# Performance work log

Hardware: AMD Instinct MI355X
Metric: run time of the kernel (lower is better)

The kernel has to match this reference:

```python
import jax, jax.numpy as jnp
import numpy as np


def _mk_mat(rows):
    # rows: list of 3 lists of (B,) arrays, written as matrix rows.
    # torch code stacks rows at dim=2, which transposes: replicate that.
    M = jnp.stack([jnp.stack(r, axis=1) for r in rows], axis=1)  # (B,3,3) written-rows
    return jnp.swapaxes(M, 1, 2)  # matches torch.stack(..., dim=2)


def _compose_mats(affine, scale, translate, shear):
    B = affine.shape[0]
    one = jnp.ones((B,), affine.dtype)
    zero = jnp.zeros((B,), affine.dtype)
    cx, sx = jnp.cos(affine[:, 0]), jnp.sin(affine[:, 0])
    cy, sy = jnp.cos(affine[:, 1]), jnp.sin(affine[:, 1])
    cz, sz = jnp.cos(affine[:, 2]), jnp.sin(affine[:, 2])
    rot_x = _mk_mat([[one, zero, zero], [zero, cx, -sx], [zero, sx, cx]])
    rot_y = _mk_mat([[cy, zero, sy], [zero, one, zero], [-sy, zero, cy]])
    rot_z = _mk_mat([[cz, -sz, zero], [sz, cz, zero], [zero, zero, one]])
    scale_m = _mk_mat([[scale[:, 0], zero, zero], [zero, scale[:, 1], zero], [zero, zero, scale[:, 2]]])
    t = jnp.tan(shear)
    shear_m = _mk_mat([[one, t[:, 0], t[:, 1]], [t[:, 2], one, t[:, 3]], [t[:, 4], t[:, 5], one]])
    trans = translate[:, :, None]  # (B,3,1)
    mat3 = shear_m @ (scale_m @ (rot_z @ (rot_y @ rot_x)))  # (B,3,3)
    inv3 = jnp.linalg.inv(mat3)
    mat = jnp.concatenate([mat3, trans], axis=-1)  # (B,3,4)
    inv_trans = jnp.matmul(-inv3, trans)
    inv_mat = jnp.concatenate([inv3, inv_trans], axis=-1)
    return mat, inv_mat


def _affine_grid(mat, D, H, W):
    # torch affine_grid, align_corners=False: coord_i = (2*i+1)/n - 1
    dt = mat.dtype
    xs = (jnp.arange(W, dtype=dt) + 0.5) * (2.0 / W) - 1.0
    ys = (jnp.arange(H, dtype=dt) + 0.5) * (2.0 / H) - 1.0
    zs = (jnp.arange(D, dtype=dt) + 0.5) * (2.0 / D) - 1.0
    zz, yy, xx = jnp.meshgrid(zs, ys, xs, indexing='ij')
    coords = jnp.stack([xx, yy, zz], axis=-1)  # (D,H,W,3) in (x,y,z) order
    grid = jnp.einsum('bkj,dhwj->bdhwk', mat[:, :, :3], coords) + mat[:, None, None, None, :, 3]
    return grid  # (B,D,H,W,3)


def _grid_sample_trilinear(src, grid):
    # torch grid_sample, mode='bilinear' (trilinear in 3D), padding zeros, align_corners=False
    B, C, D, H, W = src.shape
    ix = (grid[..., 0] + 1.0) * (W * 0.5) - 0.5
    iy = (grid[..., 1] + 1.0) * (H * 0.5) - 0.5
    iz = (grid[..., 2] + 1.0) * (D * 0.5) - 0.5
    fx, fy, fz = jnp.floor(ix), jnp.floor(iy), jnp.floor(iz)
    wx, wy, wz = ix - fx, iy - fy, iz - fz  # fractional weights
    x0, y0, z0 = fx.astype(jnp.int32), fy.astype(jnp.int32), fz.astype(jnp.int32)
    x1, y1, z1 = x0 + 1, y0 + 1, z0 + 1
    N = D * H * W
    src_flat = src.reshape(B, C, N)

    def gather(z, y, x):
        valid = (x >= 0) & (x < W) & (y >= 0) & (y < H) & (z >= 0) & (z < D)
        xi = jnp.clip(x, 0, W - 1)
        yi = jnp.clip(y, 0, H - 1)
        zi = jnp.clip(z, 0, D - 1)
        idx = ((zi * H + yi) * W + xi).reshape(B, 1, N)
        v = jnp.take_along_axis(src_flat, jnp.broadcast_to(idx, (B, C, N)), axis=2)
        return v * valid.reshape(B, 1, N).astype(src.dtype)

    def w(a):
        return a.reshape(B, 1, N)

    out = (gather(z0, y0, x0) * w((1 - wz) * (1 - wy) * (1 - wx))
           + gather(z0, y0, x1) * w((1 - wz) * (1 - wy) * wx)
           + gather(z0, y1, x0) * w((1 - wz) * wy * (1 - wx))
           + gather(z0, y1, x1) * w((1 - wz) * wy * wx)
           + gather(z1, y0, x0) * w(wz * (1 - wy) * (1 - wx))
           + gather(z1, y0, x1) * w(wz * (1 - wy) * wx)
           + gather(z1, y1, x0) * w(wz * wy * (1 - wx))
           + gather(z1, y1, x1) * w(wz * wy * wx))
    return out.reshape(B, C, D, H, W)


def setup_inputs() -> dict:
    key = jax.random.key(0)
    k1, k2, k3, k4, k5 = jax.random.split(key, 5)
    B, C, D, H, W = 2, 1, 192, 192, 192
    src = jax.random.normal(k1, (B, C, D, H, W), dtype=jnp.float32)
    affine = jax.random.uniform(k2, (B, 3), dtype=jnp.float32)
    scale = jax.random.uniform(k3, (B, 3), dtype=jnp.float32)
    translate = jax.random.uniform(k4, (B, 3), dtype=jnp.float32)
    shear = jax.random.uniform(k5, (B, 6), dtype=jnp.float32)
    return {"src": src, "affine": affine, "scale": scale, "translate": translate, "shear": shear}


def reference(src, affine, scale, translate, shear):
    B, C, D, H, W = src.shape
    mat, inv_mat = _compose_mats(affine, scale, translate, shear)
    grid = _affine_grid(mat, D, H, W)
    warped = _grid_sample_trilinear(src, grid)
    return warped, mat, inv_mat
```

## Files before the change

### kernel.cpp

```cpp
#include <hip/hip_runtime.h>
#include <math.h>

#define Bv 2
#define Dv 192
#define Hv 192
#define Wv 192
#define Nv (Dv*Hv*Wv)
#define NOUT (Bv*Nv)

#define TLZ 8
#define SWID 32
#define CAPF 13312

typedef float v2f __attribute__((ext_vector_type(2)));

__device__ __forceinline__ void mm3(const float a[3][3], const float b[3][3], float c[3][3]) {
#pragma unroll
    for (int i = 0; i < 3; ++i)
#pragma unroll
        for (int j = 0; j < 3; ++j)
            c[i][j] = a[i][0]*b[0][j] + a[i][1]*b[1][j] + a[i][2]*b[2][j];
}

__global__ void compose_mats_kernel(const float* __restrict__ affine,
                                    const float* __restrict__ scale,
                                    const float* __restrict__ translate,
                                    const float* __restrict__ shear,
                                    float* __restrict__ mats_out) {
    int b = threadIdx.x;
    if (b >= Bv) return;

    float ax = affine[b*3+0], ay = affine[b*3+1], az = affine[b*3+2];
    float cx = cosf(ax), sx = sinf(ax);
    float cy = cosf(ay), sy = sinf(ay);
    float cz = cosf(az), sz = sinf(az);

    float rx[3][3] = {{1.f,0.f,0.f},{0.f,cx,sx},{0.f,-sx,cx}};
    float ry[3][3] = {{cy,0.f,-sy},{0.f,1.f,0.f},{sy,0.f,cy}};
    float rz[3][3] = {{cz,sz,0.f},{-sz,cz,0.f},{0.f,0.f,1.f}};

    float t0 = tanf(shear[b*6+0]), t1 = tanf(shear[b*6+1]), t2 = tanf(shear[b*6+2]);
    float t3 = tanf(shear[b*6+3]), t4 = tanf(shear[b*6+4]), t5 = tanf(shear[b*6+5]);
    float sh[3][3] = {{1.f,t2,t4},{t0,1.f,t5},{t1,t3,1.f}};

    float s0 = scale[b*3+0], s1 = scale[b*3+1], s2 = scale[b*3+2];

    float m1[3][3], m2[3][3], m3s[3][3], mat3[3][3];
    mm3(ry, rx, m1);
    mm3(rz, m1, m2);
#pragma unroll
    for (int j = 0; j < 3; ++j) { m3s[0][j] = s0*m2[0][j]; m3s[1][j] = s1*m2[1][j]; m3s[2][j] = s2*m2[2][j]; }
    mm3(sh, m3s, mat3);

    float tr0 = translate[b*3+0], tr1 = translate[b*3+1], tr2 = translate[b*3+2];

    float a00 = mat3[0][0], a01 = mat3[0][1], a02 = mat3[0][2];
    float a10 = mat3[1][0], a11 = mat3[1][1], a12 = mat3[1][2];
    float a20 = mat3[2][0], a21 = mat3[2][1], a22 = mat3[2][2];
    float c00 =  (a11*a22 - a12*a21);
    float c01 = -(a10*a22 - a12*a20);
    float c02 =  (a10*a21 - a11*a20);
    float det = a00*c00 + a01*c01 + a02*c02;
    float rdet = 1.0f / det;
    float inv3[3][3];
    inv3[0][0] = c00*rdet;
    inv3[0][1] = (a02*a21 - a01*a22)*rdet;
    inv3[0][2] = (a01*a12 - a02*a11)*rdet;
    inv3[1][0] = c01*rdet;
    inv3[1][1] = (a00*a22 - a02*a20)*rdet;
    inv3[1][2] = (a02*a10 - a00*a12)*rdet;
    inv3[2][0] = c02*rdet;
    inv3[2][1] = (a01*a20 - a00*a21)*rdet;
    inv3[2][2] = (a00*a11 - a01*a10)*rdet;

    float* mo = mats_out + b*12;
#pragma unroll
    for (int i = 0; i < 3; ++i) {
        mo[i*4+0] = mat3[i][0]; mo[i*4+1] = mat3[i][1]; mo[i*4+2] = mat3[i][2];
    }
    mo[0*4+3] = tr0; mo[1*4+3] = tr1; mo[2*4+3] = tr2;

    float* io = mats_out + 24 + b*12;
#pragma unroll
    for (int i = 0; i < 3; ++i) {
        io[i*4+0] = inv3[i][0]; io[i*4+1] = inv3[i][1]; io[i*4+2] = inv3[i][2];
        io[i*4+3] = -(inv3[i][0]*tr0 + inv3[i][1]*tr1 + inv3[i][2]*tr2);
    }
}

__device__ __forceinline__ float2 ld2(const float* p) {
    float2 r;
    __builtin_memcpy(&r, p, 8);
    return r;
}

__device__ __forceinline__ void gld_lds4(const float* g, float* l) {
    __builtin_amdgcn_global_load_lds(
        (const __attribute__((address_space(1))) unsigned int*)g,
        (__attribute__((address_space(3))) unsigned int*)l, 4, 0, 0);
}

__global__ __launch_bounds__(512) void warp_kernel(const float* __restrict__ src,
                                                   const float* __restrict__ mats,
                                                   float* __restrict__ out) {
    __shared__ float stage[CAPF];

    int t   = threadIdx.x;
    int lx  = t & 15;
    int ly  = (t >> 4) & 15;
    int lzt = t >> 8;

    int W0 = blockIdx.x * 16;
    int H0 = blockIdx.y * 16;
    int zt = blockIdx.z;
    int b  = zt / (Dv/TLZ);
    int Z0 = (zt % (Dv/TLZ)) * TLZ;

    const float* M = mats + b*12;
    float m00 = M[0], m01 = M[1],  m02 = M[2],  m03 = M[3];
    float m10 = M[4], m11 = M[5],  m12 = M[6],  m13 = M[7];
    float m20 = M[8], m21 = M[9],  m22 = M[10], m23 = M[11];

    float Cx = 96.0f*(m03 - m00 - m01 - m02) + 95.5f;
    float Cy = 96.0f*(m13 - m10 - m11 - m12) + 95.5f;
    float Cz = 96.0f*(m23 - m20 - m21 - m22) + 95.5f;

    const float* sb = src + (size_t)b * Nv;

    float bcx = W0 + 8.0f, bcy = H0 + 8.0f, bcz = Z0 + 4.0f;
    float cxv = fmaf(m00, bcx, fmaf(m01, bcy, fmaf(m02, bcz, Cx)));
    float cyv = fmaf(m10, bcx, fmaf(m11, bcy, fmaf(m12, bcz, Cy)));
    float czv = fmaf(m20, bcx, fmaf(m21, bcy, fmaf(m22, bcz, Cz)));
    float hxv = 7.5f*fabsf(m00) + 7.5f*fabsf(m01) + 3.5f*fabsf(m02);
    float hyv = 7.5f*fabsf(m10) + 7.5f*fabsf(m11) + 3.5f*fabsf(m12);
    float hzv = 7.5f*fabsf(m20) + 7.5f*fabsf(m21) + 3.5f*fabsf(m22);

    int bx0 = ((int)floorf(cxv - hxv) - 1) & ~3;
    int by0 = (int)floorf(cyv - hyv) - 1;
    int bz0 = (int)floorf(czv - hzv) - 1;
    int xmax = (int)floorf(cxv + hxv) + 2;
    int ey  = (int)floorf(cyv + hyv) + 3 - by0;
    int ez  = (int)floorf(czv + hzv) + 3 - bz0;

    int nP  = (ey + 1) >> 1;
    int PST = 68*nP + 4;

    bool interior = (PST*ez <= CAPF) && (xmax - bx0 + 1 <= SWID) &&
                    (bx0 >= 0) && (bx0 + SWID   <= Wv) &&
                    (by0 >= 0) && (by0 + 2*nP   <= Hv) &&
                    (bz0 >= 0) && (bz0 + ez     <= Dv);

    int w = W0 + lx, h = H0 + ly;
    float fw = w + 0.5f, fh = h + 0.5f;
    float fz0 = Z0 + lzt*4 + 0.5f;

    float accs[4];

    if (interior) {
        int lane = t & 63;
        int wvu  = __builtin_amdgcn_readfirstlane(t >> 6);
        int lrow = lane >> 5;
        int col  = lane & 31;
        int srcb = (bz0*Hv + by0)*Wv + bx0 + lrow*Wv + col;
        for (int dz = wvu; dz < ez; dz += 8) {
            int sp = srcb + dz*(Hv*Wv);
            int lb = dz*PST;
            for (int j = 0; j < nP; ++j) {
                gld_lds4(sb + sp, &stage[lb + j*68]);
                sp += 2*Wv;
            }
        }

        float ixb = fmaf(m00, fw, fmaf(m01, fh, fmaf(m02, fz0, Cx)));
        float iyb = fmaf(m10, fw, fmaf(m11, fh, fmaf(m12, fz0, Cy)));
        float izb = fmaf(m20, fw, fmaf(m21, fh, fmaf(m22, fz0, Cz)));

        asm volatile("s_waitcnt vmcnt(0)" ::: "memory");
        __syncthreads();

#pragma unroll
        for (int zp = 0; zp < 2; ++zp) {
            float zA = (float)(2*zp), zB = (float)(2*zp + 1);
            float ixA = fmaf(m02, zA, ixb), ixB = fmaf(m02, zB, ixb);
            float iyA = fmaf(m12, zA, iyb), iyB = fmaf(m12, zB, iyb);
            float izA = fmaf(m22, zA, izb), izB = fmaf(m22, zB, izb);

            float fxA = floorf(ixA), fxB = floorf(ixB);
            float fyA = floorf(iyA), fyB = floorf(iyB);
            float fzA = floorf(izA), fzB = floorf(izB);

            v2f wx2; wx2.x = ixA - fxA; wx2.y = ixB - fxB;
            v2f wy2; wy2.x = iyA - fyA; wy2.y = iyB - fyB;
            v2f wz2; wz2.x = izA - fzA; wz2.y = izB - fzB;

            int lixA = (int)fxA - bx0, lixB = (int)fxB - bx0;
            int liyA = (int)fyA - by0, liyB = (int)fyB - by0;
            int lizA = (int)fzA - bz0, lizB = (int)fzB - bz0;

            int oddA = liyA & 1, oddB = liyB & 1;
            int o00A = lizA*PST + 34*liyA - (oddA << 1) + lixA;
            int o00B = lizB*PST + 34*liyB - (oddB << 1) + lixB;
            int o01A = o00A + 32 + (oddA << 2);
            int o01B = o00B + 32 + (oddB << 2);
            int o10A = o00A + PST, o10B = o00B + PST;
            int o11A = o01A + PST, o11B = o01B + PST;

            v2f v000; v000.x = stage[o00A];   v000.y = stage[o00B];
            v2f v001; v001.x = stage[o00A+1]; v001.y = stage[o00B+1];
            v2f v010; v010.x = stage[o01A];   v010.y = stage[o01B];
            v2f v011; v011.x = stage[o01A+1]; v011.y = stage[o01B+1];
            v2f v100; v100.x = stage[o10A];   v100.y = stage[o10B];
            v2f v101; v101.x = stage[o10A+1]; v101.y = stage[o10B+1];
            v2f v110; v110.x = stage[o11A];   v110.y = stage[o11B];
            v2f v111; v111.x = stage[o11A+1]; v111.y = stage[o11B+1];

            v2f c00 = wx2*(v001 - v000) + v000;
            v2f c01 = wx2*(v011 - v010) + v010;
            v2f c10 = wx2*(v101 - v100) + v100;
            v2f c11 = wx2*(v111 - v110) + v110;
            v2f c0  = wy2*(c01 - c00) + c00;
            v2f c1  = wy2*(c11 - c10) + c10;
            v2f r   = wz2*(c1 - c0) + c0;
            accs[2*zp]   = r.x;
            accs[2*zp+1] = r.y;
        }
    } else {
        float ixb = fmaf(m00, fw, fmaf(m01, fh, fmaf(m02, fz0, Cx)));
        float iyb = fmaf(m10, fw, fmaf(m11, fh, fmaf(m12, fz0, Cy)));
        float izb = fmaf(m20, fw, fmaf(m21, fh, fmaf(m22, fz0, Cz)));
#pragma unroll
        for (int zi = 0; zi < 4; ++zi) {
            float ix = fmaf(m02, (float)zi, ixb);
            float iy = fmaf(m12, (float)zi, iyb);
            float iz = fmaf(m22, (float)zi, izb);
            float flx = floorf(ix), fly = floorf(iy), flz = floorf(iz);
            float wx = ix - flx, wy = iy - fly, wz = iz - flz;
            int x0 = (int)flx, y0 = (int)fly, z0 = (int)flz;

            float a = 0.0f;
            bool all_in = ((unsigned)x0 < (unsigned)(Wv-1)) &
                          ((unsigned)y0 < (unsigned)(Hv-1)) &
                          ((unsigned)z0 < (unsigned)(Dv-1));
            if (all_in) {
                const float* p = sb + ((z0*Hv + y0)*Wv + x0);
                const float* q = p + Hv*Wv;
                float2 v00 = ld2(p);
                float2 v01 = ld2(p + Wv);
                float2 v10 = ld2(q);
                float2 v11 = ld2(q + Wv);
                float c00 = fmaf(wx, v00.y - v00.x, v00.x);
                float c01 = fmaf(wx, v01.y - v01.x, v01.x);
                float c10 = fmaf(wx, v10.y - v10.x, v10.x);
                float c11 = fmaf(wx, v11.y - v11.x, v11.x);
                float c0  = fmaf(wy, c01 - c00, c00);
                float c1  = fmaf(wy, c11 - c10, c10);
                a = fmaf(wz, c1 - c0, c0);
            } else {
                int x1 = x0 + 1, y1 = y0 + 1, z1 = z0 + 1;
                bool all_out = (x1 < 0) | (x0 >= Wv) | (y1 < 0) | (y0 >= Hv) | (z1 < 0) | (z0 >= Dv);
                if (!all_out) {
                    auto gather = [&](int zz, int yy, int xx) -> float {
                        bool valid = ((unsigned)xx < (unsigned)Wv) &
                                     ((unsigned)yy < (unsigned)Hv) &
                                     ((unsigned)zz < (unsigned)Dv);
                        int xi = min(max(xx, 0), Wv-1);
                        int yi = min(max(yy, 0), Hv-1);
                        int zi2 = min(max(zz, 0), Dv-1);
                        float val = sb[(zi2*Hv + yi)*Wv + xi];
                        return valid ? val : 0.0f;
                    };
                    float owx = 1.0f - wx, owy = 1.0f - wy, owz = 1.0f - wz;
                    a  = gather(z0, y0, x0) * (owz*owy*owx);
                    a += gather(z0, y0, x1) * (owz*owy*wx);
                    a += gather(z0, y1, x0) * (owz*wy*owx);
                    a += gather(z0, y1, x1) * (owz*wy*wx);
                    a += gather(z1, y0, x0) * (wz*owy*owx);
                    a += gather(z1, y0, x1) * (wz*owy*wx);
                    a += gather(z1, y1, x0) * (wz*wy*owx);
                    a += gather(z1, y1, x1) * (wz*wy*wx);
                }
            }
            accs[zi] = a;
        }
    }

#pragma unroll
    for (int zi = 0; zi < 4; ++zi) {
        int z = Z0 + lzt*4 + zi;
        __builtin_nontemporal_store(accs[zi], &out[((size_t)(b*Dv + z)*Hv + h)*Wv + w]);
    }
}

extern "C" void kernel_launch(void* const* d_in, const int* in_sizes, int n_in,
                              void* d_out, int out_size, void* d_ws, size_t ws_size,
                              hipStream_t stream) {
    const float* src       = (const float*)d_in[0];
    const float* affine    = (const float*)d_in[1];
    const float* scale     = (const float*)d_in[2];
    const float* translate = (const float*)d_in[3];
    const float* shear     = (const float*)d_in[4];

    float* out  = (float*)d_out;
    float* mats = out + NOUT;

    compose_mats_kernel<<<1, 64, 0, stream>>>(affine, scale, translate, shear, mats);

    dim3 grid(Wv/16, Hv/16, (Dv/TLZ)*Bv);
    warp_kernel<<<grid, 512, 0, stream>>>(src, mats, out);
}
```

Measured before the change: 52.05 us.

## Stage clamped source window for all tiles with per-sample LDS fallback

Instead of using the LDS-staged trilinear path only for fully interior tiles, every tile now stages a window clamped to volume bounds and capacity. Each z-pair checks wave-wide whether all samples fall inside the staged window, and falls back to direct global gathers otherwise. The goal is to let boundary and oversized tiles use the shared-memory path and avoid slow scattered global loads. In exchange it adds staging work and a wave vote for tiles that may end up using the fallback anyway.

```diff
diff --git a/kernel.cpp b/kernel.cpp
--- a/kernel.cpp
+++ b/kernel.cpp
@@ -135,71 +135,128 @@
     float hyv = 7.5f*fabsf(m10) + 7.5f*fabsf(m11) + 3.5f*fabsf(m12);
     float hzv = 7.5f*fabsf(m20) + 7.5f*fabsf(m21) + 3.5f*fabsf(m22);
 
-    int bx0 = ((int)floorf(cxv - hxv) - 1) & ~3;
-    int by0 = (int)floorf(cyv - hyv) - 1;
-    int bz0 = (int)floorf(czv - hzv) - 1;
-    int xmax = (int)floorf(cxv + hxv) + 2;
-    int ey  = (int)floorf(cyv + hyv) + 3 - by0;
-    int ez  = (int)floorf(czv + hzv) + 3 - bz0;
-
-    int nP  = (ey + 1) >> 1;
+    int xlo = (int)floorf(cxv - hxv), xhi1 = (int)floorf(cxv + hxv) + 1;
+    int ylo = (int)floorf(cyv - hyv), yhi1 = (int)floorf(cyv + hyv) + 1;
+    int zlo = (int)floorf(czv - hzv), zhi1 = (int)floorf(czv + hzv) + 1;
+
+    int bx0 = min(max(xlo, 0), Wv - SWID);
+    int ey_s = min(yhi1 - ylo + 1, 64);
+    int nP  = (ey_s + 1) >> 1;
     int PST = 68*nP + 4;
-
-    bool interior = (PST*ez <= CAPF) && (xmax - bx0 + 1 <= SWID) &&
-                    (bx0 >= 0) && (bx0 + SWID   <= Wv) &&
-                    (by0 >= 0) && (by0 + 2*nP   <= Hv) &&
-                    (bz0 >= 0) && (bz0 + ez     <= Dv);
+    int ez_need = zhi1 - zlo + 1;
+    int ez_s = min(ez_need, CAPF / PST);
+    int by0 = min(max(ylo, 0), Hv - 2*nP);
+    int bz0 = min(max(zlo + ((ez_need - ez_s) >> 1), 0), Dv - max(ez_s, 0));
+
+    bool uok = (xhi1 >= 0) & (xlo < Wv) & (yhi1 >= 0) & (ylo < Hv) &
+               (zhi1 >= 0) & (zlo < Dv) & (ez_s >= 2) & (ey_s >= 2);
+    if (!uok) ez_s = 0;
 
     int w = W0 + lx, h = H0 + ly;
     float fw = w + 0.5f, fh = h + 0.5f;
     float fz0 = Z0 + lzt*4 + 0.5f;
 
+    int lane = t & 63;
+    int wvu  = __builtin_amdgcn_readfirstlane(t >> 6);
+    int lrow = lane >> 5;
+    int col  = lane & 31;
+    int srcb = (bz0*Hv + by0)*Wv + bx0 + lrow*Wv + col;
+    for (int dz = wvu; dz < ez_s; dz += 8) {
+        int sp = srcb + dz*(Hv*Wv);
+        int lb = dz*PST;
+        for (int j = 0; j < nP; ++j) {
+            gld_lds4(sb + sp, &stage[lb + j*68]);
+            sp += 2*Wv;
+        }
+    }
+
+    float ixb = fmaf(m00, fw, fmaf(m01, fh, fmaf(m02, fz0, Cx)));
+    float iyb = fmaf(m10, fw, fmaf(m11, fh, fmaf(m12, fz0, Cy)));
+    float izb = fmaf(m20, fw, fmaf(m21, fh, fmaf(m22, fz0, Cz)));
+
+    asm volatile("s_waitcnt vmcnt(0)" ::: "memory");
+    __syncthreads();
+
+    auto direct_sample = [&](float ix, float iy, float iz) -> float {
+        float flx = floorf(ix), fly = floorf(iy), flz = floorf(iz);
+        float wx = ix - flx, wy = iy - fly, wz = iz - flz;
+        int x0 = (int)flx, y0 = (int)fly, z0 = (int)flz;
+        bool all_in = ((unsigned)x0 < (unsigned)(Wv-1)) &
+                      ((unsigned)y0 < (unsigned)(Hv-1)) &
+                      ((unsigned)z0 < (unsigned)(Dv-1));
+        if (all_in) {
+            const float* p = sb + ((z0*Hv + y0)*Wv + x0);
+            const float* q = p + Hv*Wv;
+            float2 v00 = ld2(p);
+            float2 v01 = ld2(p + Wv);
+            float2 v10 = ld2(q);
+            float2 v11 = ld2(q + Wv);
+            float c00 = fmaf(wx, v00.y - v00.x, v00.x);
+            float c01 = fmaf(wx, v01.y - v01.x, v01.x);
+            float c10 = fmaf(wx, v10.y - v10.x, v10.x);
+            float c11 = fmaf(wx, v11.y - v11.x, v11.x);
+            float c0  = fmaf(wy, c01 - c00, c00);
+            float c1  = fmaf(wy, c11 - c10, c10);
+            return fmaf(wz, c1 - c0, c0);
+        }
+        int x1 = x0 + 1, y1 = y0 + 1, z1 = z0 + 1;
+        bool all_out = (x1 < 0) | (x0 >= Wv) | (y1 < 0) | (y0 >= Hv) | (z1 < 0) | (z0 >= Dv);
+        if (all_out) return 0.0f;
+        auto gather = [&](int zz, int yy, int xx) -> float {
+            bool valid = ((unsigned)xx < (unsigned)Wv) &
+                         ((unsigned)yy < (unsigned)Hv) &
+                         ((unsigned)zz < (unsigned)Dv);
+            int xi = min(max(xx, 0), Wv-1);
+            int yi = min(max(yy, 0), Hv-1);
+            int zi = min(max(zz, 0), Dv-1);
+            float val = sb[(zi*Hv + yi)*Wv + xi];
+            return valid ? val : 0.0f;
+        };
+        float owx = 1.0f - wx, owy = 1.0f - wy, owz = 1.0f - wz;
+        float a;
+        a  = gather(z0, y0, x0) * (owz*owy*owx);
+        a += gather(z0, y0, x1) * (owz*owy*wx);
+        a += gather(z0, y1, x0) * (owz*wy*owx);
+        a += gather(z0, y1, x1) * (owz*wy*wx);
+        a += gather(z1, y0, x0) * (wz*owy*owx);
+        a += gather(z1, y0, x1) * (wz*owy*wx);
+        a += gather(z1, y1, x0) * (wz*wy*owx);
+        a += gather(z1, y1, x1) * (wz*wy*wx);
+        return a;
+    };
+
     float accs[4];
 
-    if (interior) {
-        int lane = t & 63;
-        int wvu  = __builtin_amdgcn_readfirstlane(t >> 6);
-        int lrow = lane >> 5;
-        int col  = lane & 31;
-        int srcb = (bz0*Hv + by0)*Wv + bx0 + lrow*Wv + col;
-        for (int dz = wvu; dz < ez; dz += 8) {
-            int sp = srcb + dz*(Hv*Wv);
-            int lb = dz*PST;
-            for (int j = 0; j < nP; ++j) {
-                gld_lds4(sb + sp, &stage[lb + j*68]);
-                sp += 2*Wv;
-            }
-        }
-
-        float ixb = fmaf(m00, fw, fmaf(m01, fh, fmaf(m02, fz0, Cx)));
-        float iyb = fmaf(m10, fw, fmaf(m11, fh, fmaf(m12, fz0, Cy)));
-        float izb = fmaf(m20, fw, fmaf(m21, fh, fmaf(m22, fz0, Cz)));
-
-        asm volatile("s_waitcnt vmcnt(0)" ::: "memory");
-        __syncthreads();
-
-#pragma unroll
-        for (int zp = 0; zp < 2; ++zp) {
-            float zA = (float)(2*zp), zB = (float)(2*zp + 1);
-            float ixA = fmaf(m02, zA, ixb), ixB = fmaf(m02, zB, ixb);
-            float iyA = fmaf(m12, zA, iyb), iyB = fmaf(m12, zB, iyb);
-            float izA = fmaf(m22, zA, izb), izB = fmaf(m22, zB, izb);
-
-            float fxA = floorf(ixA), fxB = floorf(ixB);
-            float fyA = floorf(iyA), fyB = floorf(iyB);
-            float fzA = floorf(izA), fzB = floorf(izB);
-
+#pragma unroll
+    for (int zp = 0; zp < 2; ++zp) {
+        float zA = (float)(2*zp), zB = (float)(2*zp + 1);
+        float ixA = fmaf(m02, zA, ixb), ixB = fmaf(m02, zB, ixb);
+        float iyA = fmaf(m12, zA, iyb), iyB = fmaf(m12, zB, iyb);
+        float izA = fmaf(m22, zA, izb), izB = fmaf(m22, zB, izb);
+
+        float fxA = floorf(ixA), fxB = floorf(ixB);
+        float fyA = floorf(iyA), fyB = floorf(iyB);
+        float fzA = floorf(izA), fzB = floorf(izB);
+
+        int dxA = (int)fxA - bx0, dxB = (int)fxB - bx0;
+        int dyA = (int)fyA - by0, dyB = (int)fyB - by0;
+        int dzA = (int)fzA - bz0, dzB = (int)fzB - bz0;
+
+        bool okA = ((unsigned)dxA <= (unsigned)(SWID-2)) &
+                   ((unsigned)dyA <= (unsigned)(ey_s-2)) &
+                   ((unsigned)dzA <= (unsigned)(ez_s-2));
+        bool okB = ((unsigned)dxB <= (unsigned)(SWID-2)) &
+                   ((unsigned)dyB <= (unsigned)(ey_s-2)) &
+                   ((unsigned)dzB <= (unsigned)(ez_s-2));
+
+        if (uok && __all(okA & okB)) {
             v2f wx2; wx2.x = ixA - fxA; wx2.y = ixB - fxB;
             v2f wy2; wy2.x = iyA - fyA; wy2.y = iyB - fyB;
             v2f wz2; wz2.x = izA - fzA; wz2.y = izB - fzB;
 
-            int lixA = (int)fxA - bx0, lixB = (int)fxB - bx0;
-            int liyA = (int)fyA - by0, liyB = (int)fyB - by0;
-            int lizA = (int)fzA - bz0, lizB = (int)fzB - bz0;
-
-            int oddA = liyA & 1, oddB = liyB & 1;
-            int o00A = lizA*PST + 34*liyA - (oddA << 1) + lixA;
-            int o00B = lizB*PST + 34*liyB - (oddB << 1) + lixB;
+            int oddA = dyA & 1, oddB = dyB & 1;
+            int o00A = dzA*PST + 34*dyA - (oddA << 1) + dxA;
+            int o00B = dzB*PST + 34*dyB - (oddB << 1) + dxB;
             int o01A = o00A + 32 + (oddA << 2);
             int o01B = o00B + 32 + (oddB << 2);
             int o10A = o00A + PST, o10B = o00B + PST;
@@ -223,64 +280,9 @@
             v2f r   = wz2*(c1 - c0) + c0;
             accs[2*zp]   = r.x;
             accs[2*zp+1] = r.y;
-        }
-    } else {
-        float ixb = fmaf(m00, fw, fmaf(m01, fh, fmaf(m02, fz0, Cx)));
-        float iyb = fmaf(m10, fw, fmaf(m11, fh, fmaf(m12, fz0, Cy)));
-        float izb = fmaf(m20, fw, fmaf(m21, fh, fmaf(m22, fz0, Cz)));
-#pragma unroll
-        for (int zi = 0; zi < 4; ++zi) {
-            float ix = fmaf(m02, (float)zi, ixb);
-            float iy = fmaf(m12, (float)zi, iyb);
-            float iz = fmaf(m22, (float)zi, izb);
-            float flx = floorf(ix), fly = floorf(iy), flz = floorf(iz);
-            float wx = ix - flx, wy = iy - fly, wz = iz - flz;
-            int x0 = (int)flx, y0 = (int)fly, z0 = (int)flz;
-
-            float a = 0.0f;
-            bool all_in = ((unsigned)x0 < (unsigned)(Wv-1)) &
-                          ((unsigned)y0 < (unsigned)(Hv-1)) &
-                          ((unsigned)z0 < (unsigned)(Dv-1));
-            if (all_in) {
-                const float* p = sb + ((z0*Hv + y0)*Wv + x0);
-                const float* q = p + Hv*Wv;
-                float2 v00 = ld2(p);
-                float2 v01 = ld2(p + Wv);
-                float2 v10 = ld2(q);
-                float2 v11 = ld2(q + Wv);
-                float c00 = fmaf(wx, v00.y - v00.x, v00.x);
-                float c01 = fmaf(wx, v01.y - v01.x, v01.x);
-                float c10 = fmaf(wx, v10.y - v10.x, v10.x);
-                float c11 = fmaf(wx, v11.y - v11.x, v11.x);
-                float c0  = fmaf(wy, c01 - c00, c00);
-                float c1  = fmaf(wy, c11 - c10, c10);
-                a = fmaf(wz, c1 - c0, c0);
-            } else {
-                int x1 = x0 + 1, y1 = y0 + 1, z1 = z0 + 1;
-                bool all_out = (x1 < 0) | (x0 >= Wv) | (y1 < 0) | (y0 >= Hv) | (z1 < 0) | (z0 >= Dv);
-                if (!all_out) {
-                    auto gather = [&](int zz, int yy, int xx) -> float {
-                        bool valid = ((unsigned)xx < (unsigned)Wv) &
-                                     ((unsigned)yy < (unsigned)Hv) &
-                                     ((unsigned)zz < (unsigned)Dv);
-                        int xi = min(max(xx, 0), Wv-1);
-                        int yi = min(max(yy, 0), Hv-1);
-                        int zi2 = min(max(zz, 0), Dv-1);
-                        float val = sb[(zi2*Hv + yi)*Wv + xi];
-                        return valid ? val : 0.0f;
-                    };
-                    float owx = 1.0f - wx, owy = 1.0f - wy, owz = 1.0f - wz;
-                    a  = gather(z0, y0, x0) * (owz*owy*owx);
-                    a += gather(z0, y0, x1) * (owz*owy*wx);
-                    a += gather(z0, y1, x0) * (owz*wy*owx);
-                    a += gather(z0, y1, x1) * (owz*wy*wx);
-                    a += gather(z1, y0, x0) * (wz*owy*owx);
-                    a += gather(z1, y0, x1) * (wz*owy*wx);
-                    a += gather(z1, y1, x0) * (wz*wy*owx);
-                    a += gather(z1, y1, x1) * (wz*wy*wx);
-                }
-            }
-            accs[zi] = a;
+        } else {
+            accs[2*zp]   = direct_sample(ixA, iyA, izA);
+            accs[2*zp+1] = direct_sample(ixB, iyB, izB);
         }
     }
 
```

New measurement: 50.97 us. 2.1% less time.
